# Performance work log

Hardware: AMD Instinct MI355X
Metric: run time of the kernel (lower is better)

The kernel has to match this reference:

```python
import jax, jax.numpy as jnp
import numpy as np
from jax.scipy.special import erf

B, S, D = 8, 512, 512
H = 8            # num_heads per half
DH = D // 2      # 256, per-branch model dim
DFF = 2048
HOUT = 2


def _layernorm(x, g, b, eps=1e-6):
    mu = jnp.mean(x, axis=-1, keepdims=True)
    var = jnp.mean(jnp.square(x - mu), axis=-1, keepdims=True)
    return (x - mu) / jnp.sqrt(var + eps) * g + b


def _rescale_dist(w):
    one = jnp.float32(1.0)
    return (one + jnp.exp(one)) / (one + jnp.exp(one - w))


def _mha(xin, wq, bq, wk, bk, wv, bv, wo, bo, maskf, adjoin, dist):
    b, s, dm = xin.shape
    dep = dm // H
    def heads(t):
        return t.reshape(b, s, H, dep).transpose(0, 2, 1, 3)  # (b,h,s,dep)
    q = heads(xin @ wq + bq)
    k = heads(xin @ wk + bk)
    v = heads(xin @ wv + bv)
    scores = jnp.einsum('bhqd,bhkd->bhqk', q, k)
    scale = jnp.sqrt(jnp.float32(dep))
    if dist is not None:
        scores = jax.nn.relu(scores) * _rescale_dist(dist) / scale
    else:
        scores = scores / scale
    scores = scores + maskf * jnp.float32(-1e9)
    if adjoin is not None:
        scores = scores + adjoin
    attn = jax.nn.softmax(scores, axis=-1)
    out = jnp.einsum('bhqk,bhkd->bhqd', attn, v).transpose(0, 2, 1, 3).reshape(b, s, dm)
    return out @ wo + bo, attn


def setup_inputs() -> dict:
    key = jax.random.key(0)
    ks = jax.random.split(key, 32)
    init = lambda k, shp: (jax.random.normal(k, shp, dtype=jnp.float32) * 0.02)
    inp = {
        'x': jax.random.normal(ks[0], (B, S, D), dtype=jnp.float32),
        'adjoin_matrix': jax.random.normal(ks[1], (B, 1, S, S), dtype=jnp.float32),
        'dist_matrix': jax.random.uniform(ks[2], (B, 1, S, S), dtype=jnp.float32),
        # mha1 (adjoin branch)
        'wq1': init(ks[3], (DH, DH)), 'bq1': jnp.zeros((DH,), jnp.float32),
        'wk1': init(ks[4], (DH, DH)), 'bk1': jnp.zeros((DH,), jnp.float32),
        'wv1': init(ks[5], (DH, DH)), 'bv1': jnp.zeros((DH,), jnp.float32),
        'wo1': init(ks[6], (DH, DH)), 'bo1': jnp.zeros((DH,), jnp.float32),
        # mha2 (distance branch)
        'wq2': init(ks[7], (DH, DH)), 'bq2': jnp.zeros((DH,), jnp.float32),
        'wk2': init(ks[8], (DH, DH)), 'bk2': jnp.zeros((DH,), jnp.float32),
        'wv2': init(ks[9], (DH, DH)), 'bv2': jnp.zeros((DH,), jnp.float32),
        'wo2': init(ks[10], (DH, DH)), 'bo2': jnp.zeros((DH,), jnp.float32),
        # BANLayer
        'vnet_w': init(ks[11], (DH, 2 * DH)), 'vnet_b': jnp.zeros((2 * DH,), jnp.float32),
        'qnet_w': init(ks[12], (DH, 2 * DH)), 'qnet_b': jnp.zeros((2 * DH,), jnp.float32),
        'h_mat': init(ks[13], (1, HOUT, 1, 2 * DH)),
        'h_bias': init(ks[14], (1, HOUT, 1, 1)),
        'bn_gamma': jnp.ones((D,), jnp.float32), 'bn_beta': jnp.zeros((D,), jnp.float32),
        'bn_mean': jnp.zeros((D,), jnp.float32), 'bn_var': jnp.ones((D,), jnp.float32),
        # LayerNorms
        'ln1_g': jnp.ones((D,), jnp.float32), 'ln1_b': jnp.zeros((D,), jnp.float32),
        'ln2_g': jnp.ones((D,), jnp.float32), 'ln2_b': jnp.zeros((D,), jnp.float32),
        # FFN
        'ffn_w1': init(ks[15], (D, DFF)), 'ffn_b1': jnp.zeros((DFF,), jnp.float32),
        'ffn_w2': init(ks[16], (DFF, D)), 'ffn_b2': jnp.zeros((D,), jnp.float32),
        # padding mask (int -> cast), 1 = masked
        'encoder_padding_mask': jax.random.randint(ks[17], (B, 1, 1, S), 0, 2, dtype=jnp.int32),
    }
    return inp


def reference(x, adjoin_matrix, dist_matrix,
              wq1, bq1, wk1, bk1, wv1, bv1, wo1, bo1,
              wq2, bq2, wk2, bk2, wv2, bv2, wo2, bo2,
              vnet_w, vnet_b, qnet_w, qnet_b, h_mat, h_bias,
              bn_gamma, bn_beta, bn_mean, bn_var,
              ln1_g, ln1_b, ln2_g, ln2_b,
              ffn_w1, ffn_b1, ffn_w2, ffn_b2,
              encoder_padding_mask):
    maskf = encoder_padding_mask.astype(jnp.float32)
    x1, x2 = jnp.split(x, 2, axis=-1)
    # local branch: adjoin bias, no distance
    x_l, aw_local = _mha(x1, wq1, bq1, wk1, bk1, wv1, bv1, wo1, bo1, maskf, adjoin_matrix, None)
    # global branch: relu + distance rescale, no adjoin
    x_g, aw_global = _mha(x2, wq2, bq2, wk2, bk2, wv2, bv2, wo2, bo2, maskf, None, dist_matrix)
    # BANLayer (h_out=2 <= c, eval mode; p_net is identity for rows=1)
    v_ = jax.nn.relu(x_l @ vnet_w + vnet_b)   # (B,S,2*DH)
    q_ = jax.nn.relu(x_g @ qnet_w + qnet_b)
    att_maps = jnp.einsum('xhyk,bvk,bqk->bhvq', h_mat, v_, q_) + h_bias  # (B,HOUT,S,S)
    logits = jnp.einsum('bvk,bhvq,bqk->bvk', v_, att_maps, q_)           # sum over h
    logits = (logits - bn_mean) / jnp.sqrt(bn_var + 1e-3) * bn_gamma + bn_beta
    attn_output = logits * jnp.concatenate([x_l, x_g], axis=-1)
    out1 = _layernorm(x + attn_output, ln1_g, ln1_b)
    h = out1 @ ffn_w1 + ffn_b1
    h = 0.5 * h * (1.0 + erf(h / jnp.sqrt(jnp.float32(2.0))))  # exact gelu
    ffn_out = h @ ffn_w2 + ffn_b2
    out2 = _layernorm(out1 + ffn_out, ln2_g, ln2_b)
    return (out2, aw_local, aw_global)
```

## Files before the change

kernel.cpp:

```cpp
#include <hip/hip_runtime.h>
#include <hip/hip_bf16.h>

typedef __hip_bfloat16 bf16;
typedef __attribute__((ext_vector_type(8))) short bf16x8;
typedef __attribute__((ext_vector_type(4))) float f32x4;

#define BB 8
#define SS 512
#define DD 512
#define NH 8
#define DHm 256
#define DFF 2048

__device__ __forceinline__ void gl_lds16(const void* g, void* l) {
  __builtin_amdgcn_global_load_lds((const __attribute__((address_space(1))) void*)g,
                                   (__attribute__((address_space(3))) void*)l, 16, 0, 0);
}

__device__ __forceinline__ bf16x8 cvt8(const float* p) {
  union { bf16x8 v; bf16 h[8]; } u;
  float4 f0 = *(const float4*)p, f1 = *(const float4*)(p + 4);
  u.h[0]=__float2bfloat16(f0.x); u.h[1]=__float2bfloat16(f0.y);
  u.h[2]=__float2bfloat16(f0.z); u.h[3]=__float2bfloat16(f0.w);
  u.h[4]=__float2bfloat16(f1.x); u.h[5]=__float2bfloat16(f1.y);
  u.h[6]=__float2bfloat16(f1.z); u.h[7]=__float2bfloat16(f1.w);
  return u.v;
}

template<int BM, int BN, int SMODE, int BIASM, int ACT>
__global__ __launch_bounds__(256)
void gemm2(const bf16* __restrict__ A, const bf16* __restrict__ B,
           const float* __restrict__ bias, float* __restrict__ Cf,
           bf16* __restrict__ Cb, int K, int lda, int ldb, int ldc,
           long long sA, long long sB, long long sC, int sBias)
{
  __shared__ bf16 As[BM * 32];
  __shared__ bf16 Bs[BN * 32];
  const int t = threadIdx.x, lane = t & 63, wave = t >> 6;
  const int l15 = lane & 15, quad = lane >> 4;
  constexpr int WMT = BM / 32, WNT = BN / 32;
  const int wm = (wave & 1) * (BM / 2), wn = (wave >> 1) * (BN / 2);
  const int row0 = blockIdx.y * BM, col0 = blockIdx.x * BN;
  const bf16* Ab = A + (long long)blockIdx.z * sA + (long long)row0 * lda;
  const bf16* Bb = B + (long long)blockIdx.z * sB + (long long)col0 * ldb;
  const int srow = wave * 16 + (lane >> 2), skc = (lane & 3) << 3;

  f32x4 acc[WMT][WNT] = {};

  for (int k0 = 0; k0 < K; k0 += 32) {
#pragma unroll
    for (int j = 0; j < BM / 64; j++)
      gl_lds16(Ab + (long long)(srow + j * 64) * lda + k0 + skc,
               (char*)As + wave * 1024 + j * 4096);
#pragma unroll
    for (int j = 0; j < BN / 64; j++)
      gl_lds16(Bb + (long long)(srow + j * 64) * ldb + k0 + skc,
               (char*)Bs + wave * 1024 + j * 4096);
    __syncthreads();
    bf16x8 af[WMT], bfr[WNT];
#pragma unroll
    for (int i = 0; i < WMT; i++) af[i]  = *(const bf16x8*)&As[(wm + i * 16 + l15) * 32 + quad * 8];
#pragma unroll
    for (int j = 0; j < WNT; j++) bfr[j] = *(const bf16x8*)&Bs[(wn + j * 16 + l15) * 32 + quad * 8];
#pragma unroll
    for (int i = 0; i < WMT; i++)
#pragma unroll
      for (int j = 0; j < WNT; j++)
        acc[i][j] = __builtin_amdgcn_mfma_f32_16x16x32_bf16(af[i], bfr[j], acc[i][j], 0, 0, 0);
    __syncthreads();
  }

  float sb = 0.f;
  if (BIASM == 2) sb = bias[0] + bias[1];
#pragma unroll
  for (int i = 0; i < WMT; i++)
#pragma unroll
    for (int j = 0; j < WNT; j++) {
      int col = col0 + wn + j * 16 + l15;
      float bv = (BIASM == 1) ? bias[(long long)blockIdx.z * sBias + col] : sb;
#pragma unroll
      for (int r = 0; r < 4; r++) {
        int row = row0 + wm + i * 16 + (quad << 2) + r;
        float v = acc[i][j][r] + bv;
        if (ACT == 1) v = fmaxf(v, 0.f);
        if (ACT == 2) v = 0.5f * v * (1.f + erff(v * 0.70710678118654752f));
        long long ci = (long long)blockIdx.z * sC + (long long)row * ldc + col;
        if (SMODE & 1) Cf[ci] = v;
        if (SMODE & 2) Cb[ci] = __float2bfloat16(v);
      }
    }
}

__global__ __launch_bounds__(256, 2)
void attn_fused(const bf16* __restrict__ QKV1, const bf16* __restrict__ QKV2,
                const int* __restrict__ mask,
                const float* __restrict__ adjoin, const float* __restrict__ dist,
                float* __restrict__ awl, float* __restrict__ awg,
                bf16* __restrict__ ctx1, bf16* __restrict__ ctx2)
{
  const int qt = blockIdx.x, h = blockIdx.y, zz = blockIdx.z;
  const int b = zz & 7, branch = zz >> 3;
  const bf16* __restrict__ QKV = branch ? QKV2 : QKV1;
  const float* __restrict__ extra = branch ? dist : adjoin;
  float* __restrict__ aw = branch ? awg : awl;
  bf16* __restrict__ ctx = branch ? ctx2 : ctx1;

  const int t = threadIdx.x, lane = t & 63, wave = t >> 6;
  const int l15 = lane & 15, quad = lane >> 4;
  __shared__ bf16x8 Vt[64][32];
  alignas(16) __shared__ bf16 Pl[4][2][2048];

  {
    const bf16* Vb = QKV + (long long)b * SS * 768 + 512 + h * 32;
    int dep = t & 31;
#pragma unroll
    for (int j8 = 0; j8 < 8; j8++) {
      int blk = (t >> 5) + (j8 << 3);
      union { bf16x8 v; bf16 hh[8]; } u;
#pragma unroll
      for (int i = 0; i < 8; i++)
        u.hh[i] = Vb[(long long)(blk * 8 + i) * 768 + dep];
      Vt[blk][dep] = u.v;
    }
  }

  const int q0 = qt * 64 + wave * 16;
  const bf16* Qb = QKV + ((long long)(b * SS + q0)) * 768 + h * 32;
  bf16x8 qfrag = *(const bf16x8*)(Qb + (long long)l15 * 768 + quad * 8);
  __syncthreads();

  const float scale_inv = 0.17677669529663688f;
  const bf16* Kb = QKV + (long long)b * SS * 768 + 256 + h * 32;
  const float* Eb = extra + ((long long)b * SS + q0) * SS;
  float sreg[32][4];
  float rmax[4] = {-1e30f, -1e30f, -1e30f, -1e30f};
#pragma unroll
  for (int kc = 0; kc < 32; kc++) {
    int kpos = kc * 16 + l15;
    bf16x8 kfrag = *(const bf16x8*)(Kb + (long long)kpos * 768 + quad * 8);
    f32x4 a = __builtin_amdgcn_mfma_f32_16x16x32_bf16(qfrag, kfrag, f32x4{0.f,0.f,0.f,0.f}, 0, 0, 0);
    float mval = (float)mask[b * SS + kpos] * -1e9f;
#pragma unroll
    for (int r = 0; r < 4; r++) {
      float s = a[r];
      float ev = Eb[(long long)(quad * 4 + r) * SS + kpos];
      if (branch == 0) {
        s = s * scale_inv + mval + ev;
      } else {
        float resc = 3.7182818284590452f / (1.f + __expf(1.f - ev));
        s = fmaxf(s, 0.f) * resc * scale_inv + mval;
      }
      sreg[kc][r] = s;
      rmax[r] = fmaxf(rmax[r], s);
    }
  }
#pragma unroll
  for (int r = 0; r < 4; r++) {
    float v = rmax[r];
    v = fmaxf(v, __shfl_xor(v, 1, 16));
    v = fmaxf(v, __shfl_xor(v, 2, 16));
    v = fmaxf(v, __shfl_xor(v, 4, 16));
    v = fmaxf(v, __shfl_xor(v, 8, 16));
    rmax[r] = v;
  }
  float rsum[4] = {0.f, 0.f, 0.f, 0.f};
#pragma unroll
  for (int kc = 0; kc < 32; kc++)
#pragma unroll
    for (int r = 0; r < 4; r++) {
      float e = __expf(sreg[kc][r] - rmax[r]);
      sreg[kc][r] = e;
      rsum[r] += e;
    }
#pragma unroll
  for (int r = 0; r < 4; r++) {
    float v = rsum[r];
    v += __shfl_xor(v, 1, 16);
    v += __shfl_xor(v, 2, 16);
    v += __shfl_xor(v, 4, 16);
    v += __shfl_xor(v, 8, 16);
    rsum[r] = 1.f / v;
  }

  float* awp = aw + (((long long)(b * NH + h) * SS + q0)) * SS;
#pragma unroll
  for (int kc = 0; kc < 32; kc++)
#pragma unroll
    for (int r = 0; r < 4; r++) {
      float p = sreg[kc][r] * rsum[r];
      sreg[kc][r] = p;
      __builtin_nontemporal_store(p, awp + (long long)(quad * 4 + r) * SS + kc * 16 + l15);
    }

  f32x4 oacc[2] = {};
  const int rkey = ((l15 >> 2) ^ l15) & 3;
#pragma unroll
  for (int c = 0; c < 4; c++) {
    bf16* Pw = Pl[wave][c & 1];
#pragma unroll
    for (int kcl = 0; kcl < 8; kcl++)
#pragma unroll
      for (int r = 0; r < 4; r++) {
        const int key = (quad ^ r) & 3;
        const int off = (quad * 4 + r) * 256 + (((kcl * 16 + l15) * 2) ^ (key << 5));
        *(bf16*)((char*)Pw + off) = __float2bfloat16(sreg[c * 8 + kcl][r]);
      }
    asm volatile("s_waitcnt lgkmcnt(0)" ::: "memory");
    __builtin_amdgcn_s_setprio(1);
#pragma unroll
    for (int k2 = 0; k2 < 4; k2++) {
      const int off = l15 * 256 + ((k2 * 64 + quad * 16) ^ (rkey << 5));
      bf16x8 afr = *(const bf16x8*)((const char*)Pw + off);
      const int blk = (c * 4 + k2) * 4 + quad;
      oacc[0] = __builtin_amdgcn_mfma_f32_16x16x32_bf16(afr, Vt[blk][l15],      oacc[0], 0, 0, 0);
      oacc[1] = __builtin_amdgcn_mfma_f32_16x16x32_bf16(afr, Vt[blk][16 + l15], oacc[1], 0, 0, 0);
    }
    __builtin_amdgcn_s_setprio(0);
  }

#pragma unroll
  for (int n = 0; n < 2; n++)
#pragma unroll
    for (int r = 0; r < 4; r++) {
      int q = q0 + quad * 4 + r;
      ctx[(long long)(b * SS + q) * DHm + h * 32 + n * 16 + l15] = __float2bfloat16(oacc[n][r]);
    }
}

__device__ __forceinline__ void tr_tile(const float* __restrict__ src, bf16* __restrict__ dst,
                                        int K, int N, int tile) {
  __shared__ float tl[32][33];
  int tilesN = N >> 5;
  int tk = tile / tilesN, tn = tile % tilesN;
  int c = threadIdx.x & 31, r0 = threadIdx.x >> 5;
#pragma unroll
  for (int i = 0; i < 4; i++) {
    int r = r0 + i * 8;
    tl[r][c] = src[(long long)(tk * 32 + r) * N + tn * 32 + c];
  }
  __syncthreads();
#pragma unroll
  for (int i = 0; i < 4; i++) {
    int r = r0 + i * 8;
    dst[(long long)(tn * 32 + r) * K + tk * 32 + c] = __float2bfloat16(tl[c][r]);
  }
}

__global__ __launch_bounds__(256)
void pack_all(const float* wq1, const float* wk1, const float* wv1,
              const float* wq2, const float* wk2, const float* wv2,
              const float* wo1, const float* wo2,
              const float* vnet_w, const float* qnet_w,
              const float* ffn_w1, const float* ffn_w2,
              const float* bq1, const float* bk1, const float* bv1,
              const float* bq2, const float* bk2, const float* bv2,
              const float* bo1, const float* bo2,
              const float* vnet_b, const float* qnet_b,
              const float* x,
              bf16* WB1, bf16* WB2, bf16* woT1, bf16* woT2,
              bf16* vnetT, bf16* qnetT, bf16* f1T, bf16* f2T,
              float* BB1v, float* BB2v, float* BOv, float* VQb, bf16* xb)
{
  int blk = blockIdx.x;
  if (blk < 64)        { tr_tile(wq1, WB1,            256, 256, blk); return; }
  if (blk < 128)       { tr_tile(wk1, WB1 + 256*256,  256, 256, blk-64); return; }
  if (blk < 192)       { tr_tile(wv1, WB1 + 512*256,  256, 256, blk-128); return; }
  if (blk < 256)       { tr_tile(wq2, WB2,            256, 256, blk-192); return; }
  if (blk < 320)       { tr_tile(wk2, WB2 + 256*256,  256, 256, blk-256); return; }
  if (blk < 384)       { tr_tile(wv2, WB2 + 512*256,  256, 256, blk-320); return; }
  if (blk < 448)       { tr_tile(wo1, woT1,           256, 256, blk-384); return; }
  if (blk < 512)       { tr_tile(wo2, woT2,           256, 256, blk-448); return; }
  if (blk < 640)       { tr_tile(vnet_w, vnetT,       256, 512, blk-512); return; }
  if (blk < 768)       { tr_tile(qnet_w, qnetT,       256, 512, blk-640); return; }
  if (blk < 1792)      { tr_tile(ffn_w1, f1T,         512, 2048, blk-768); return; }
  if (blk < 2816)      { tr_tile(ffn_w2, f2T,         2048, 512, blk-1792); return; }
  if (blk < 3840) {
    long long i0 = (long long)(blk - 2816) * 2048 + threadIdx.x * 8;
    *(bf16x8*)(xb + i0) = cvt8(x + i0);
    return;
  }
  if (blk < 3846) {
    int b = blk - 3840;
    const float* src = b==0?bq1 : b==1?bk1 : b==2?bv1 : b==3?bq2 : b==4?bk2 : bv2;
    float* dst = (b < 3 ? BB1v : BB2v) + (b % 3) * 256;
    dst[threadIdx.x] = src[threadIdx.x];
    return;
  }
  if (blk < 3848) {
    int b = blk - 3846;
    BOv[b * 256 + threadIdx.x] = (b ? bo2 : bo1)[threadIdx.x];
    return;
  }
  {
    int b = blk - 3848;
    const float* src = (b < 2) ? vnet_b : qnet_b;
    VQb[b * 256 + threadIdx.x] = src[(b & 1) * 256 + threadIdx.x];
  }
}

__global__ __launch_bounds__(256)
void tr_qn(const bf16* __restrict__ Qn, bf16* __restrict__ QnT)
{
  int b = blockIdx.z, tk = blockIdx.y, tn = blockIdx.x;
  __shared__ bf16 tl[32][33];
  int c = threadIdx.x & 31, r0 = threadIdx.x >> 5;
  const bf16* src = Qn + (long long)b * 512 * 512;
  bf16* dst = QnT + (long long)b * 512 * 512;
#pragma unroll
  for (int i = 0; i < 4; i++) { int r = r0 + i * 8; tl[r][c] = src[(tk * 32 + r) * 512 + tn * 32 + c]; }
  __syncthreads();
#pragma unroll
  for (int i = 0; i < 4; i++) { int r = r0 + i * 8; dst[(tn * 32 + r) * 512 + tk * 32 + c] = tl[c][r]; }
}

__global__ __launch_bounds__(256)
void vh_kernel(const bf16* __restrict__ v_, const float* __restrict__ hmat,
               bf16* __restrict__ vh, int n)
{
  int i = blockIdx.x * 256 + threadIdx.x;
  if (i < n) {
    int c = i & (DD - 1);
    vh[i] = __float2bfloat16(__bfloat162float(v_[i]) * (hmat[c] + hmat[DD + c]));
  }
}

__global__ __launch_bounds__(256)
void bn_gate_ln1_kernel(const float* __restrict__ x, const bf16* __restrict__ vbuf,
                        const float* __restrict__ T, const float* __restrict__ xl,
                        const float* __restrict__ xg,
                        const float* __restrict__ bng, const float* __restrict__ bnb,
                        const float* __restrict__ bnm, const float* __restrict__ bnv,
                        const float* __restrict__ lng, const float* __restrict__ lnb,
                        float* __restrict__ out1, bf16* __restrict__ out1b)
{
  const int row = blockIdx.x;
  const int t = threadIdx.x;
  const int lane = t & 63, wave = t >> 6;
  __shared__ float red[8];
  float val[2];
#pragma unroll
  for (int i = 0; i < 2; i++) {
    int c = t + i * 256;
    long long idx = (long long)row * DD + c;
    float lg = __bfloat162float(vbuf[idx]) * T[idx];
    float bn = (lg - bnm[c]) / sqrtf(bnv[c] + 1e-3f) * bng[c] + bnb[c];
    float gate = (c < DHm) ? xl[(long long)row * DHm + c] : xg[(long long)row * DHm + (c - DHm)];
    val[i] = x[idx] + bn * gate;
  }
  float s = val[0] + val[1];
#pragma unroll
  for (int o = 32; o > 0; o >>= 1) s += __shfl_xor(s, o);
  if (lane == 0) red[wave] = s;
  __syncthreads();
  float mu = (red[0] + red[1] + red[2] + red[3]) * (1.f / 512.f);
  float d0 = val[0] - mu, d1 = val[1] - mu;
  float vs = d0 * d0 + d1 * d1;
#pragma unroll
  for (int o = 32; o > 0; o >>= 1) vs += __shfl_xor(vs, o);
  if (lane == 0) red[4 + wave] = vs;
  __syncthreads();
  float inv = 1.f / sqrtf((red[4] + red[5] + red[6] + red[7]) * (1.f / 512.f) + 1e-6f);
  float o0 = d0 * inv * lng[t] + lnb[t];
  float o1 = d1 * inv * lng[t + 256] + lnb[t + 256];
  out1[(long long)row * DD + t] = o0;
  out1[(long long)row * DD + t + 256] = o1;
  out1b[(long long)row * DD + t] = __float2bfloat16(o0);
  out1b[(long long)row * DD + t + 256] = __float2bfloat16(o1);
}

__global__ __launch_bounds__(256)
void ln2_kernel(const float* __restrict__ a, const float* __restrict__ b2,
                const float* __restrict__ g, const float* __restrict__ bta,
                float* __restrict__ out)
{
  const int row = blockIdx.x;
  const int t = threadIdx.x;
  const int lane = t & 63, wave = t >> 6;
  __shared__ float red[8];
  float v0 = a[(long long)row * DD + t]       + b2[(long long)row * DD + t];
  float v1 = a[(long long)row * DD + t + 256] + b2[(long long)row * DD + t + 256];
  float s = v0 + v1;
#pragma unroll
  for (int o = 32; o > 0; o >>= 1) s += __shfl_xor(s, o);
  if (lane == 0) red[wave] = s;
  __syncthreads();
  float mu = (red[0] + red[1] + red[2] + red[3]) * (1.f / 512.f);
  float d0 = v0 - mu, d1 = v1 - mu;
  float vs = d0 * d0 + d1 * d1;
#pragma unroll
  for (int o = 32; o > 0; o >>= 1) vs += __shfl_xor(vs, o);
  if (lane == 0) red[4 + wave] = vs;
  __syncthreads();
  float inv = 1.f / sqrtf((red[4] + red[5] + red[6] + red[7]) * (1.f / 512.f) + 1e-6f);
  out[(long long)row * DD + t]       = d0 * inv * g[t]       + bta[t];
  out[(long long)row * DD + t + 256] = d1 * inv * g[t + 256] + bta[t + 256];
}

extern "C" void kernel_launch(void* const* d_in, const int* in_sizes, int n_in,
                              void* d_out, int out_size, void* d_ws, size_t ws_size,
                              hipStream_t stream) {
  const float* x      = (const float*)d_in[0];
  const float* adjoin = (const float*)d_in[1];
  const float* dist   = (const float*)d_in[2];
  const float* wq1=(const float*)d_in[3],  *bq1=(const float*)d_in[4];
  const float* wk1=(const float*)d_in[5],  *bk1=(const float*)d_in[6];
  const float* wv1=(const float*)d_in[7],  *bv1=(const float*)d_in[8];
  const float* wo1=(const float*)d_in[9],  *bo1=(const float*)d_in[10];
  const float* wq2=(const float*)d_in[11], *bq2=(const float*)d_in[12];
  const float* wk2=(const float*)d_in[13], *bk2=(const float*)d_in[14];
  const float* wv2=(const float*)d_in[15], *bv2=(const float*)d_in[16];
  const float* wo2=(const float*)d_in[17], *bo2=(const float*)d_in[18];
  const float* vnet_w=(const float*)d_in[19], *vnet_b=(const float*)d_in[20];
  const float* qnet_w=(const float*)d_in[21], *qnet_b=(const float*)d_in[22];
  const float* h_mat=(const float*)d_in[23], *h_bias=(const float*)d_in[24];
  const float* bn_g=(const float*)d_in[25], *bn_b=(const float*)d_in[26];
  const float* bn_m=(const float*)d_in[27], *bn_v=(const float*)d_in[28];
  const float* ln1_g=(const float*)d_in[29], *ln1_b=(const float*)d_in[30];
  const float* ln2_g=(const float*)d_in[31], *ln2_b=(const float*)d_in[32];
  const float* ffn_w1=(const float*)d_in[33], *ffn_b1=(const float*)d_in[34];
  const float* ffn_w2=(const float*)d_in[35], *ffn_b2=(const float*)d_in[36];
  const int* mask = (const int*)d_in[37];

  char* base = (char*)d_ws;
  size_t off = 0;
  auto alloc = [&](size_t bytes) { char* p = base + off; off += (bytes + 255) & ~(size_t)255; return p; };
  bf16*  xb    = (bf16*) alloc(4096LL*512*2);
  bf16*  WB1   = (bf16*) alloc(768*256*2);
  bf16*  WB2   = (bf16*) alloc(768*256*2);
  float* BB1v  = (float*)alloc(768*4);
  float* BB2v  = (float*)alloc(768*4);
  float* BOv   = (float*)alloc(512*4);
  float* VQb   = (float*)alloc(1024*4);
  bf16*  woT1  = (bf16*) alloc(256*256*2);
  bf16*  woT2  = (bf16*) alloc(256*256*2);
  bf16*  vnetT = (bf16*) alloc(512*256*2);
  bf16*  qnetT = (bf16*) alloc(512*256*2);
  bf16*  f1T   = (bf16*) alloc(2048*512*2);
  bf16*  f2T   = (bf16*) alloc(512*2048*2);
  bf16*  QKV1  = (bf16*) alloc(4096LL*768*2);
  bf16*  QKV2  = (bf16*) alloc(4096LL*768*2);
  bf16*  CTX   = (bf16*) alloc(4096LL*256*2);
  bf16*  CTX2  = (bf16*) alloc(4096LL*256*2);
  float* XL    = (float*)alloc(4096LL*256*4);
  float* XG    = (float*)alloc(4096LL*256*4);
  bf16*  XLb   = (bf16*) alloc(4096LL*256*2);
  bf16*  XGb   = (bf16*) alloc(4096LL*256*2);
  bf16*  Vn    = (bf16*) alloc(4096LL*512*2);
  bf16*  Qn    = (bf16*) alloc(4096LL*512*2);
  bf16*  QnT   = (bf16*) alloc(4096LL*512*2);
  bf16*  VH    = (bf16*) alloc(4096LL*512*2);
  bf16*  G     = (bf16*) alloc(8LL*512*512*2);
  float* T     = (float*)alloc(4096LL*512*4);
  float* OUT1  = (float*)alloc(4096LL*512*4);
  bf16*  OUT1b = (bf16*) alloc(4096LL*512*2);
  bf16*  H     = (bf16*) alloc(4096LL*2048*2);
  float* FFNO  = (float*)alloc(4096LL*512*4);

  float* out2 = (float*)d_out;
  float* awl  = out2 + 2097152LL;
  float* awg  = awl + 16777216LL;

  const int MR = BB * SS;
  const long long GST = (long long)SS * SS;

  pack_all<<<dim3(3852), 256, 0, stream>>>(
      wq1, wk1, wv1, wq2, wk2, wv2, wo1, wo2, vnet_w, qnet_w, ffn_w1, ffn_w2,
      bq1, bk1, bv1, bq2, bk2, bv2, bo1, bo2, vnet_b, qnet_b, x,
      WB1, WB2, woT1, woT2, vnetT, qnetT, f1T, f2T, BB1v, BB2v, BOv, VQb, xb);

  gemm2<128,128,2,1,0><<<dim3(6, 32, 2), 256, 0, stream>>>(
      xb, WB1, BB1v, nullptr, QKV1, 256, 512, 256, 768,
      256LL, 768LL*256, 4096LL*768, 768);

  attn_fused<<<dim3(8, NH, 16), 256, 0, stream>>>(
      QKV1, QKV2, mask, adjoin, dist, awl, awg, CTX, CTX2);

  gemm2<64,64,3,1,0><<<dim3(4, 64, 2), 256, 0, stream>>>(
      CTX, woT1, BOv, XL, XLb, 256, 256, 256, 256,
      4096LL*256, 256LL*256, 4096LL*256, 256);

  gemm2<64,64,2,1,1><<<dim3(8, 64, 2), 256, 0, stream>>>(
      XLb, vnetT, VQb, nullptr, Vn, 256, 256, 256, 512,
      4096LL*256, 512LL*256, 4096LL*512, 512);

  vh_kernel<<<dim3((MR * DD) / 256), 256, 0, stream>>>(Vn, h_mat, VH, MR * DD);
  tr_qn<<<dim3(16, 16, BB), 256, 0, stream>>>(Qn, QnT);
  gemm2<64,64,2,2,0><<<dim3(8, 8, BB), 256, 0, stream>>>(
      VH, Qn, h_bias, nullptr, G, 512, 512, 512, 512, GST, GST, GST, 0);
  gemm2<64,64,1,0,0><<<dim3(8, 8, BB), 256, 0, stream>>>(
      G, QnT, nullptr, T, nullptr, 512, 512, 512, 512, GST, GST, GST, 0);

  bn_gate_ln1_kernel<<<dim3(MR), 256, 0, stream>>>(
      x, Vn, T, XL, XG, bn_g, bn_b, bn_m, bn_v, ln1_g, ln1_b, OUT1, OUT1b);

  gemm2<128,128,2,1,2><<<dim3(16, 32, 1), 256, 0, stream>>>(
      OUT1b, f1T, ffn_b1, nullptr, H, 512, 512, 512, 2048, 0, 0, 0, 0);
  gemm2<64,128,1,1,0><<<dim3(4, 64, 1), 256, 0, stream>>>(
      H, f2T, ffn_b2, FFNO, nullptr, 2048, 2048, 2048, 512, 0, 0, 0, 0);

  ln2_kernel<<<dim3(MR), 256, 0, stream>>>(OUT1, FFNO, ln2_g, ln2_b, out2);
}
```

Baseline: 483.6 us.

## Fuse softmax exp with PV accumulation, dropping max pass and deferring normalization

The attention kernel now computes exp(score) directly, without subtracting the row max. It writes the bf16 exp values to LDS and accumulates P·V chunk by chunk during the score loop, then normalizes both the context and the attention-weight outputs by the row sum at the end. The unnormalized exps are kept packed as bf16 pairs in registers instead of 128 fp32 scores, which frees registers and halves the P LDS buffer, so launch bounds go from 2 to 3 blocks per SM. This removes one full pass and the max reduction. In exchange, it risks overflow for large scores and NaN for fully masked rows, and the attention-weight outputs lose precision because they are now derived from bf16-rounded exps.

```diff
diff --git a/kernel.cpp b/kernel.cpp
--- a/kernel.cpp
+++ b/kernel.cpp
@@ -4,6 +4,8 @@
 typedef __hip_bfloat16 bf16;
 typedef __attribute__((ext_vector_type(8))) short bf16x8;
 typedef __attribute__((ext_vector_type(4))) float f32x4;
+typedef unsigned int u32;
+typedef unsigned short u16;
 
 #define BB 8
 #define SS 512
@@ -91,7 +93,7 @@
     }
 }
 
-__global__ __launch_bounds__(256, 2)
+__global__ __launch_bounds__(256, 3)
 void attn_fused(const bf16* __restrict__ QKV1, const bf16* __restrict__ QKV2,
                 const int* __restrict__ mask,
                 const float* __restrict__ adjoin, const float* __restrict__ dist,
@@ -108,7 +110,7 @@
   const int t = threadIdx.x, lane = t & 63, wave = t >> 6;
   const int l15 = lane & 15, quad = lane >> 4;
   __shared__ bf16x8 Vt[64][32];
-  alignas(16) __shared__ bf16 Pl[4][2][2048];
+  alignas(16) __shared__ bf16 Pl[4][2048];
 
   {
     const bf16* Vb = QKV + (long long)b * SS * 768 + 512 + h * 32;
@@ -132,46 +134,61 @@
   const float scale_inv = 0.17677669529663688f;
   const bf16* Kb = QKV + (long long)b * SS * 768 + 256 + h * 32;
   const float* Eb = extra + ((long long)b * SS + q0) * SS;
-  float sreg[32][4];
-  float rmax[4] = {-1e30f, -1e30f, -1e30f, -1e30f};
-#pragma unroll
-  for (int kc = 0; kc < 32; kc++) {
-    int kpos = kc * 16 + l15;
-    bf16x8 kfrag = *(const bf16x8*)(Kb + (long long)kpos * 768 + quad * 8);
-    f32x4 a = __builtin_amdgcn_mfma_f32_16x16x32_bf16(qfrag, kfrag, f32x4{0.f,0.f,0.f,0.f}, 0, 0, 0);
-    float mval = (float)mask[b * SS + kpos] * -1e9f;
-#pragma unroll
-    for (int r = 0; r < 4; r++) {
-      float s = a[r];
-      float ev = Eb[(long long)(quad * 4 + r) * SS + kpos];
-      if (branch == 0) {
-        s = s * scale_inv + mval + ev;
-      } else {
-        float resc = 3.7182818284590452f / (1.f + __expf(1.f - ev));
-        s = fmaxf(s, 0.f) * resc * scale_inv + mval;
+
+  u32 ehist[64];
+  float rsum[4] = {0.f, 0.f, 0.f, 0.f};
+  f32x4 oacc[2] = {};
+  bf16* Pw = Pl[wave];
+  const int rkey = ((l15 >> 2) ^ l15) & 3;
+
+#pragma unroll
+  for (int c = 0; c < 4; c++) {
+#pragma unroll
+    for (int kcl = 0; kcl < 8; kcl++) {
+      const int kc = c * 8 + kcl;
+      const int kpos = kc * 16 + l15;
+      bf16x8 kfrag = *(const bf16x8*)(Kb + (long long)kpos * 768 + quad * 8);
+      f32x4 a = __builtin_amdgcn_mfma_f32_16x16x32_bf16(qfrag, kfrag, f32x4{0.f,0.f,0.f,0.f}, 0, 0, 0);
+      float mval = (float)mask[b * SS + kpos] * -1e9f;
+      u32 p01 = 0, p23 = 0;
+#pragma unroll
+      for (int r = 0; r < 4; r++) {
+        float s = a[r];
+        float ev = Eb[(long long)(quad * 4 + r) * SS + kpos];
+        if (branch == 0) {
+          s = s * scale_inv + mval + ev;
+        } else {
+          float resc = 3.7182818284590452f / (1.f + __expf(1.f - ev));
+          s = fmaxf(s, 0.f) * resc * scale_inv + mval;
+        }
+        float e = __expf(s);
+        rsum[r] += e;
+        bf16 ebh = __float2bfloat16(e);
+        u16 us = *(u16*)&ebh;
+        if (r == 0)      p01 = us;
+        else if (r == 1) p01 |= (u32)us << 16;
+        else if (r == 2) p23 = us;
+        else             p23 |= (u32)us << 16;
+        const int key = (quad ^ r) & 3;
+        const int off = (quad * 4 + r) * 256 + (((kcl * 16 + l15) * 2) ^ (key << 5));
+        *(bf16*)((char*)Pw + off) = ebh;
       }
-      sreg[kc][r] = s;
-      rmax[r] = fmaxf(rmax[r], s);
-    }
-  }
-#pragma unroll
-  for (int r = 0; r < 4; r++) {
-    float v = rmax[r];
-    v = fmaxf(v, __shfl_xor(v, 1, 16));
-    v = fmaxf(v, __shfl_xor(v, 2, 16));
-    v = fmaxf(v, __shfl_xor(v, 4, 16));
-    v = fmaxf(v, __shfl_xor(v, 8, 16));
-    rmax[r] = v;
-  }
-  float rsum[4] = {0.f, 0.f, 0.f, 0.f};
-#pragma unroll
-  for (int kc = 0; kc < 32; kc++)
-#pragma unroll
-    for (int r = 0; r < 4; r++) {
-      float e = __expf(sreg[kc][r] - rmax[r]);
-      sreg[kc][r] = e;
-      rsum[r] += e;
-    }
+      ehist[kc * 2]     = p01;
+      ehist[kc * 2 + 1] = p23;
+    }
+    __builtin_amdgcn_s_setprio(1);
+#pragma unroll
+    for (int k2 = 0; k2 < 4; k2++) {
+      const int off = l15 * 256 + ((k2 * 64 + quad * 16) ^ (rkey << 5));
+      bf16x8 afr = *(const bf16x8*)((const char*)Pw + off);
+      const int blk = (c * 4 + k2) * 4 + quad;
+      oacc[0] = __builtin_amdgcn_mfma_f32_16x16x32_bf16(afr, Vt[blk][l15],      oacc[0], 0, 0, 0);
+      oacc[1] = __builtin_amdgcn_mfma_f32_16x16x32_bf16(afr, Vt[blk][16 + l15], oacc[1], 0, 0, 0);
+    }
+    __builtin_amdgcn_s_setprio(0);
+  }
+
+  float rsi[4];
 #pragma unroll
   for (int r = 0; r < 4; r++) {
     float v = rsum[r];
@@ -179,43 +196,21 @@
     v += __shfl_xor(v, 2, 16);
     v += __shfl_xor(v, 4, 16);
     v += __shfl_xor(v, 8, 16);
-    rsum[r] = 1.f / v;
+    rsi[r] = 1.f / v;
   }
 
   float* awp = aw + (((long long)(b * NH + h) * SS + q0)) * SS;
 #pragma unroll
-  for (int kc = 0; kc < 32; kc++)
+  for (int kc = 0; kc < 32; kc++) {
+    u32 p01 = ehist[kc * 2], p23 = ehist[kc * 2 + 1];
 #pragma unroll
     for (int r = 0; r < 4; r++) {
-      float p = sreg[kc][r] * rsum[r];
-      sreg[kc][r] = p;
-      __builtin_nontemporal_store(p, awp + (long long)(quad * 4 + r) * SS + kc * 16 + l15);
-    }
-
-  f32x4 oacc[2] = {};
-  const int rkey = ((l15 >> 2) ^ l15) & 3;
-#pragma unroll
-  for (int c = 0; c < 4; c++) {
-    bf16* Pw = Pl[wave][c & 1];
-#pragma unroll
-    for (int kcl = 0; kcl < 8; kcl++)
-#pragma unroll
-      for (int r = 0; r < 4; r++) {
-        const int key = (quad ^ r) & 3;
-        const int off = (quad * 4 + r) * 256 + (((kcl * 16 + l15) * 2) ^ (key << 5));
-        *(bf16*)((char*)Pw + off) = __float2bfloat16(sreg[c * 8 + kcl][r]);
-      }
-    asm volatile("s_waitcnt lgkmcnt(0)" ::: "memory");
-    __builtin_amdgcn_s_setprio(1);
-#pragma unroll
-    for (int k2 = 0; k2 < 4; k2++) {
-      const int off = l15 * 256 + ((k2 * 64 + quad * 16) ^ (rkey << 5));
-      bf16x8 afr = *(const bf16x8*)((const char*)Pw + off);
-      const int blk = (c * 4 + k2) * 4 + quad;
-      oacc[0] = __builtin_amdgcn_mfma_f32_16x16x32_bf16(afr, Vt[blk][l15],      oacc[0], 0, 0, 0);
-      oacc[1] = __builtin_amdgcn_mfma_f32_16x16x32_bf16(afr, Vt[blk][16 + l15], oacc[1], 0, 0, 0);
-    }
-    __builtin_amdgcn_s_setprio(0);
+      u32 bits = (r == 0) ? (p01 & 0xffffu) : (r == 1) ? (p01 >> 16)
+               : (r == 2) ? (p23 & 0xffffu) : (p23 >> 16);
+      float e = __uint_as_float(bits << 16);
+      __builtin_nontemporal_store(e * rsi[r],
+          awp + (long long)(quad * 4 + r) * SS + kc * 16 + l15);
+    }
   }
 
 #pragma unroll
@@ -223,7 +218,8 @@
 #pragma unroll
     for (int r = 0; r < 4; r++) {
       int q = q0 + quad * 4 + r;
-      ctx[(long long)(b * SS + q) * DHm + h * 32 + n * 16 + l15] = __float2bfloat16(oacc[n][r]);
+      ctx[(long long)(b * SS + q) * DHm + h * 32 + n * 16 + l15] =
+          __float2bfloat16(oacc[n][r] * rsi[r]);
     }
 }
 
```

Measured after the change: 565.1 us. 16.9% more time.
